# Kernel tuning notes

Measured on AMD Instinct MI355X. Metric: run time of the kernel, lower is better.

The kernel has to match this reference:

```python
import jax, jax.numpy as jnp
import numpy as np

NEG_INF = -1e30  # mask value used by QANet's apply_mask


def setup_inputs() -> dict:
    key = jax.random.key(0)
    ks = jax.random.split(key, 6)
    B, C, Q, H = 64, 1024, 128, 512
    return {
        "x_context": jax.random.normal(ks[0], (B, C, H), dtype=jnp.float32),
        "x_query": jax.random.normal(ks[1], (B, Q, H), dtype=jnp.float32),
        "context_mask": jnp.ones((B, C), dtype=jnp.float32),
        "query_mask": jnp.ones((B, Q), dtype=jnp.float32),
        "W0": jax.random.normal(ks[2], (H,), dtype=jnp.float32) * 0.05,
        "W1": jax.random.normal(ks[3], (H,), dtype=jnp.float32) * 0.05,
        "W2": jax.random.normal(ks[4], (H,), dtype=jnp.float32) * 0.05,
        "bias": jnp.zeros((1,), dtype=jnp.float32),
    }


def reference(x_context, x_query, context_mask, query_mask, W0, W1, W2, bias):
    # Trilinear similarity S[b,c,q] = q.W0 + c.W1 + (q*W2).c + bias
    # (original computes [B,Q,C] then transposes; we build [B,C,Q] directly)
    sub0 = jnp.einsum('bqh,h->bq', x_query, W0)          # [B,Q]
    sub1 = jnp.einsum('bch,h->bc', x_context, W1)        # [B,C]
    sub2 = jnp.einsum('bch,bqh->bcq', x_context, x_query * W2)  # [B,C,Q]
    S = sub2 + sub1[:, :, None] + sub0[:, None, :] + bias  # [B,C,Q]

    mq = query_mask[:, None, :]    # [B,1,Q]
    mc = context_mask[:, :, None]  # [B,C,1]

    # context-to-query: softmax over query axis, masked by query_mask
    S_ = jax.nn.softmax(S + (1.0 - mq) * NEG_INF, axis=-1)  # [B,C,Q]
    c2q = jnp.einsum('bcq,bqh->bch', S_, x_query)           # [B,C,H]

    # query-to-context: softmax over context axis, masked by context_mask
    S_c = jax.nn.softmax(S + (1.0 - mc) * NEG_INF, axis=1)  # [B,C,Q]
    S_T = jnp.swapaxes(S_c, 1, 2)                            # [B,Q,C]
    # (S_ @ S_T) @ x_context, associated as S_ @ (S_T @ x_context)
    tmp = jnp.einsum('bqc,bch->bqh', S_T, x_context)        # [B,Q,H]
    q2c = jnp.einsum('bcq,bqh->bch', S_, tmp)               # [B,C,H]
    return c2q, q2c
```

## Files before the change

### kernel.cpp

```cpp
#include <hip/hip_runtime.h>

#define BB 64
#define CC 1024
#define QQ 128
#define HH 512

typedef short bf16x8 __attribute__((ext_vector_type(8)));
typedef float f32x4 __attribute__((ext_vector_type(4)));

#define GLD16(g, l)                                                            \
    __builtin_amdgcn_global_load_lds(                                          \
        (const __attribute__((address_space(1))) unsigned int*)(g),            \
        (__attribute__((address_space(3))) unsigned int*)(l), 16, 0, 0)

__device__ __forceinline__ unsigned short f2bf(float f) {
    unsigned u = __float_as_uint(f);
    u += 0x7FFF + ((u >> 16) & 1);
    return (unsigned short)(u >> 16);
}
__device__ __forceinline__ unsigned pk2(float lo, float hi) {
    return (unsigned)f2bf(lo) | ((unsigned)f2bf(hi) << 16);
}

__global__ __launch_bounds__(256) void k_sub0(const float* __restrict__ xq,
                                              const float* __restrict__ w0,
                                              float* __restrict__ sub0,
                                              float* __restrict__ colsum) {
    if (blockIdx.x < 32) colsum[blockIdx.x * 256 + threadIdx.x] = 0.0f;
    int wave = threadIdx.x >> 6;
    int lane = threadIdx.x & 63;
    int row  = blockIdx.x * 4 + wave;
    const float* p = xq + (size_t)row * HH + lane * 8;
    float4 a0 = *(const float4*)(p);
    float4 a1 = *(const float4*)(p + 4);
    float4 b0 = *(const float4*)(w0 + lane * 8);
    float4 b1 = *(const float4*)(w0 + lane * 8 + 4);
    float s = a0.x*b0.x + a0.y*b0.y + a0.z*b0.z + a0.w*b0.w
            + a1.x*b1.x + a1.y*b1.y + a1.z*b1.z + a1.w*b1.w;
    #pragma unroll
    for (int off = 32; off; off >>= 1) s += __shfl_xor(s, off);
    if (lane == 0) sub0[row] = s;
}

__global__ __launch_bounds__(256) void k_prep(const float* __restrict__ xq,
                                              const float* __restrict__ w2,
                                              const float* __restrict__ qmask,
                                              unsigned short* __restrict__ xqw2b,
                                              unsigned short* __restrict__ xqmT) {
    int b  = blockIdx.y;
    int ht = blockIdx.x * 128;
    int tid = threadIdx.x;
    __shared__ __align__(16) unsigned short sT[128][132];

    {
        int q  = tid >> 1;
        int hh = (tid & 1) * 64;
        float qm = qmask[b * QQ + q];
        const float* xp = xq + ((size_t)b * QQ + q) * HH + ht + hh;
        unsigned short* wr = xqw2b + ((size_t)b * QQ + q) * HH + ht + hh;
        #pragma unroll
        for (int i = 0; i < 16; i++) {
            float4 v = *(const float4*)(xp + i * 4);
            float4 w = *(const float4*)(w2 + ht + hh + i * 4);
            uint2 pw; pw.x = pk2(v.x * w.x, v.y * w.y);
                      pw.y = pk2(v.z * w.z, v.w * w.w);
            *(uint2*)(wr + i * 4) = pw;
            uint2 pm; pm.x = pk2(v.x * qm, v.y * qm);
                      pm.y = pk2(v.z * qm, v.w * qm);
            *(uint2*)(&sT[q][hh + i * 4]) = pm;
        }
    }
    __syncthreads();
    {
        int h  = tid >> 1;
        int qh = (tid & 1) * 64;
        unsigned short* orow = xqmT + ((size_t)b * HH + ht + h) * QQ + qh;
        #pragma unroll
        for (int i = 0; i < 8; i++) {
            uint4 o;
            o.x = (unsigned)sT[qh + i*8 + 0][h] | ((unsigned)sT[qh + i*8 + 1][h] << 16);
            o.y = (unsigned)sT[qh + i*8 + 2][h] | ((unsigned)sT[qh + i*8 + 3][h] << 16);
            o.z = (unsigned)sT[qh + i*8 + 4][h] | ((unsigned)sT[qh + i*8 + 5][h] << 16);
            o.w = (unsigned)sT[qh + i*8 + 6][h] | ((unsigned)sT[qh + i*8 + 7][h] << 16);
            *(uint4*)(orow + i * 8) = o;
        }
    }
}

__global__ __launch_bounds__(256) void k_scores(
    const float* __restrict__ xc, const unsigned short* __restrict__ xqw2b,
    const float* __restrict__ w1, const float* __restrict__ cmask,
    const float* __restrict__ qmask, const float* __restrict__ bias,
    const float* __restrict__ sub0, unsigned short* __restrict__ Ebf,
    float* __restrict__ rowsum, float* __restrict__ colsum) {
    int b  = blockIdx.y;
    int c0 = blockIdx.x * 128;
    int tid  = threadIdx.x;
    int lane = tid & 63, wave = tid >> 6;
    int quad = lane >> 4, lcol = lane & 15;
    int wrow = (wave >> 1) * 64, wcol = (wave & 1) * 64;

    __shared__ __align__(16) unsigned short sA[128][32];
    __shared__ __align__(16) unsigned short sB[128][32];
    __shared__ float sW1[512];
    __shared__ float sSub1[128];
    __shared__ float sS0[128], sQm[128], sCm[128];
    __shared__ float sRowP[2][128], sColP[2][128];

    sW1[tid] = w1[tid]; sW1[tid + 256] = w1[tid + 256];
    if (tid < 128) {
        sS0[tid] = sub0[b * QQ + tid] + bias[0];
        sQm[tid] = qmask[b * QQ + tid];
        sCm[tid] = cmask[b * CC + c0 + tid];
    }

    f32x4 acc[4][4];
    #pragma unroll
    for (int i = 0; i < 4; i++)
        #pragma unroll
        for (int j = 0; j < 4; j++) acc[i][j] = (f32x4)0.0f;
    float s1 = 0.0f;

    int arow = tid >> 1, akh = (tid & 1) * 16;

    for (int k0 = 0; k0 < HH; k0 += 32) {
        __syncthreads();
        {
            const float* gp = xc + ((size_t)(b * CC + c0 + arow)) * HH + k0 + akh;
            float4 v0 = *(const float4*)(gp);
            float4 v1 = *(const float4*)(gp + 4);
            float4 v2 = *(const float4*)(gp + 8);
            float4 v3 = *(const float4*)(gp + 12);
            const float* wp = sW1 + k0 + akh;
            s1 += v0.x*wp[0] + v0.y*wp[1] + v0.z*wp[2] + v0.w*wp[3]
                + v1.x*wp[4] + v1.y*wp[5] + v1.z*wp[6] + v1.w*wp[7]
                + v2.x*wp[8] + v2.y*wp[9] + v2.z*wp[10] + v2.w*wp[11]
                + v3.x*wp[12] + v3.y*wp[13] + v3.z*wp[14] + v3.w*wp[15];
            uint4 p0, p1;
            p0.x = pk2(v0.x, v0.y); p0.y = pk2(v0.z, v0.w);
            p0.z = pk2(v1.x, v1.y); p0.w = pk2(v1.z, v1.w);
            p1.x = pk2(v2.x, v2.y); p1.y = pk2(v2.z, v2.w);
            p1.z = pk2(v3.x, v3.y); p1.w = pk2(v3.z, v3.w);
            *(uint4*)&sA[arow][akh]     = p0;
            *(uint4*)&sA[arow][akh + 8] = p1;
        }
        #pragma unroll
        for (int j = 0; j < 2; j++) {
            int chunk = wave * 2 + j;
            int row = chunk * 16 + (lane >> 2);
            GLD16(xqw2b + ((size_t)b * QQ + row) * HH + k0 + (lane & 3) * 8,
                  (unsigned short*)sB + chunk * 512);
        }
        __syncthreads();
        bf16x8 af[4];
        #pragma unroll
        for (int mi = 0; mi < 4; mi++)
            af[mi] = *(const bf16x8*)&sA[wrow + mi * 16 + lcol][quad * 8];
        #pragma unroll
        for (int ni = 0; ni < 4; ni++) {
            bf16x8 bfr = *(const bf16x8*)&sB[wcol + ni * 16 + lcol][quad * 8];
            #pragma unroll
            for (int mi = 0; mi < 4; mi++)
                acc[mi][ni] = __builtin_amdgcn_mfma_f32_16x16x32_bf16(
                    af[mi], bfr, acc[mi][ni], 0, 0, 0);
        }
    }

    s1 += __shfl_xor(s1, 1);
    if ((tid & 1) == 0) sSub1[arow] = s1;
    __syncthreads();

    float rsp[4][4];
    float csp[4] = {0.f, 0.f, 0.f, 0.f};
    #pragma unroll
    for (int mi = 0; mi < 4; mi++)
        #pragma unroll
        for (int r = 0; r < 4; r++) rsp[mi][r] = 0.f;

    #pragma unroll
    for (int mi = 0; mi < 4; mi++) {
        #pragma unroll
        for (int ni = 0; ni < 4; ni++) {
            int col = wcol + ni * 16 + lcol;
            float qm = sQm[col], s0 = sS0[col];
            #pragma unroll
            for (int r = 0; r < 4; r++) {
                int row = wrow + mi * 16 + quad * 4 + r;
                float e = __expf(acc[mi][ni][r] + sSub1[row] + s0);
                acc[mi][ni][r] = e;
                rsp[mi][r] += e * qm;
                csp[ni] += e * sCm[row];
            }
        }
    }
    #pragma unroll
    for (int mi = 0; mi < 4; mi++)
        #pragma unroll
        for (int r = 0; r < 4; r++) {
            float v = rsp[mi][r];
            v += __shfl_xor(v, 1); v += __shfl_xor(v, 2);
            v += __shfl_xor(v, 4); v += __shfl_xor(v, 8);
            if (lcol == 0) sRowP[wave & 1][wrow + mi * 16 + quad * 4 + r] = v;
        }
    #pragma unroll
    for (int ni = 0; ni < 4; ni++) {
        float v = csp[ni];
        v += __shfl_xor(v, 16); v += __shfl_xor(v, 32);
        if (quad == 0) sColP[wave >> 1][wcol + ni * 16 + lcol] = v;
    }
    #pragma unroll
    for (int mi = 0; mi < 4; mi++)
        #pragma unroll
        for (int ni = 0; ni < 4; ni++) {
            int col = wcol + ni * 16 + lcol;
            #pragma unroll
            for (int r = 0; r < 4; r++) {
                int row = wrow + mi * 16 + quad * 4 + r;
                Ebf[((size_t)(b * CC + c0 + row)) * QQ + col] = f2bf(acc[mi][ni][r]);
            }
        }
    __syncthreads();
    if (tid < 128) {
        rowsum[(size_t)b * CC + c0 + tid] = sRowP[0][tid] + sRowP[1][tid];
        atomicAdd(&colsum[b * QQ + tid], sColP[0][tid] + sColP[1][tid]);
    }
}

__global__ __launch_bounds__(256) void k_tmp(
    const unsigned short* __restrict__ Ebf, const float* __restrict__ xc,
    const float* __restrict__ cmask, const float* __restrict__ qmask,
    const float* __restrict__ colsum, unsigned short* __restrict__ tmpT) {
    int b  = blockIdx.y;
    int h0 = blockIdx.x * 64;
    int tid  = threadIdx.x;
    int lane = tid & 63, wave = tid >> 6;
    int quad = lane >> 4, lcol = lane & 15;
    int wrow = (wave >> 1) * 64;
    int wcol = (wave & 1) * 32;

    __shared__ __align__(16) unsigned int sAu[128 * 16];
    __shared__ __align__(16) unsigned int sBu[64 * 16];
    __shared__ float sInv[128];
    if (tid < 128) sInv[tid] = qmask[b * QQ + tid] / colsum[b * QQ + tid];

    f32x4 acc[4][2];
    #pragma unroll
    for (int i = 0; i < 4; i++) { acc[i][0] = (f32x4)0.f; acc[i][1] = (f32x4)0.f; }

    int tp = tid >> 4;
    int tq = tid & 15;

    for (int c0 = 0; c0 < CC; c0 += 32) {
        __syncthreads();
        {
            const unsigned short* ep = Ebf + ((size_t)b * CC + c0 + 2 * tp) * QQ + tq * 8;
            union { uint4 v; unsigned short s[8]; } r0, r1;
            r0.v = *(const uint4*)ep;
            r1.v = *(const uint4*)(ep + QQ);
            #pragma unroll
            for (int j = 0; j < 8; j++) {
                int q = tq * 8 + j;
                unsigned pk = (unsigned)r0.s[j] | ((unsigned)r1.s[j] << 16);
                sAu[q * 16 + (((tp >> 2) ^ (q >> 3 & 3)) << 2) + (tp & 3)] = pk;
            }
        }
        {
            const float* xp = xc + ((size_t)b * CC + c0 + 2 * tp) * HH + h0 + tq * 4;
            float cm0 = cmask[b * CC + c0 + 2 * tp];
            float cm1 = cmask[b * CC + c0 + 2 * tp + 1];
            float4 f0 = *(const float4*)xp;
            float4 f1 = *(const float4*)(xp + HH);
            float a0[4] = {f0.x, f0.y, f0.z, f0.w};
            float a1[4] = {f1.x, f1.y, f1.z, f1.w};
            #pragma unroll
            for (int j = 0; j < 4; j++) {
                int h = tq * 4 + j;
                unsigned pk = pk2(a0[j] * cm0, a1[j] * cm1);
                sBu[h * 16 + (((tp >> 2) ^ (h >> 3 & 3)) << 2) + (tp & 3)] = pk;
            }
        }
        __syncthreads();
        bf16x8 af[4];
        #pragma unroll
        for (int mi = 0; mi < 4; mi++) {
            int m = wrow + mi * 16 + lcol;
            af[mi] = *(const bf16x8*)(sAu + m * 16 + ((quad ^ (m >> 3 & 3)) << 2));
        }
        #pragma unroll
        for (int ni = 0; ni < 2; ni++) {
            int n = wcol + ni * 16 + lcol;
            bf16x8 bfr = *(const bf16x8*)(sBu + n * 16 + ((quad ^ (n >> 3 & 3)) << 2));
            #pragma unroll
            for (int mi = 0; mi < 4; mi++)
                acc[mi][ni] = __builtin_amdgcn_mfma_f32_16x16x32_bf16(
                    af[mi], bfr, acc[mi][ni], 0, 0, 0);
        }
    }
    #pragma unroll
    for (int mi = 0; mi < 4; mi++) {
        int qb = wrow + mi * 16 + quad * 4;
        #pragma unroll
        for (int ni = 0; ni < 2; ni++) {
            int h = wcol + ni * 16 + lcol;
            uint2 o;
            o.x = pk2(acc[mi][ni][0] * sInv[qb + 0], acc[mi][ni][1] * sInv[qb + 1]);
            o.y = pk2(acc[mi][ni][2] * sInv[qb + 2], acc[mi][ni][3] * sInv[qb + 3]);
            *(uint2*)(tmpT + ((size_t)b * HH + h0 + h) * QQ + qb) = o;
        }
    }
}

__global__ __launch_bounds__(256) void k_out(
    const unsigned short* __restrict__ Ebf, const unsigned short* __restrict__ xqmT,
    const unsigned short* __restrict__ tmpT, const float* __restrict__ rowsum,
    float* __restrict__ c2q, float* __restrict__ q2c) {
    int b  = blockIdx.z;
    int c0 = blockIdx.y * 128;
    int h0 = blockIdx.x * 128;
    int tid  = threadIdx.x;
    int lane = tid & 63, wave = tid >> 6;
    int quad = lane >> 4, lcol = lane & 15;
    int wrow = (wave >> 1) * 64, wcol = (wave & 1) * 64;

    __shared__ __align__(16) unsigned short sA[128][32];
    __shared__ __align__(16) unsigned short sB1[128][32];
    __shared__ __align__(16) unsigned short sB2[128][32];
    __shared__ float sInvR[128];
    if (tid < 128) sInvR[tid] = 1.0f / rowsum[(size_t)b * CC + c0 + tid];

    f32x4 acc1[4][4], acc2[4][4];
    #pragma unroll
    for (int i = 0; i < 4; i++)
        #pragma unroll
        for (int j = 0; j < 4; j++) { acc1[i][j] = (f32x4)0.f; acc2[i][j] = (f32x4)0.f; }

    for (int k0 = 0; k0 < QQ; k0 += 32) {
        __syncthreads();
        #pragma unroll
        for (int j = 0; j < 2; j++) {
            int chunk = wave * 2 + j;
            int row = chunk * 16 + (lane >> 2);
            int kb  = (lane & 3) * 8;
            GLD16(Ebf  + ((size_t)b * CC + c0 + row) * QQ + k0 + kb,
                  (unsigned short*)sA + chunk * 512);
            GLD16(xqmT + ((size_t)b * HH + h0 + row) * QQ + k0 + kb,
                  (unsigned short*)sB1 + chunk * 512);
            GLD16(tmpT + ((size_t)b * HH + h0 + row) * QQ + k0 + kb,
                  (unsigned short*)sB2 + chunk * 512);
        }
        __syncthreads();
        bf16x8 af[4];
        #pragma unroll
        for (int mi = 0; mi < 4; mi++)
            af[mi] = *(const bf16x8*)&sA[wrow + mi * 16 + lcol][quad * 8];
        #pragma unroll
        for (int ni = 0; ni < 4; ni++) {
            bf16x8 b1 = *(const bf16x8*)&sB1[wcol + ni * 16 + lcol][quad * 8];
            bf16x8 b2 = *(const bf16x8*)&sB2[wcol + ni * 16 + lcol][quad * 8];
            #pragma unroll
            for (int mi = 0; mi < 4; mi++) {
                acc1[mi][ni] = __builtin_amdgcn_mfma_f32_16x16x32_bf16(
                    af[mi], b1, acc1[mi][ni], 0, 0, 0);
                acc2[mi][ni] = __builtin_amdgcn_mfma_f32_16x16x32_bf16(
                    af[mi], b2, acc2[mi][ni], 0, 0, 0);
            }
        }
    }
    #pragma unroll
    for (int mi = 0; mi < 4; mi++) {
        int rb = wrow + mi * 16 + quad * 4;
        float ir0 = sInvR[rb], ir1 = sInvR[rb + 1], ir2 = sInvR[rb + 2], ir3 = sInvR[rb + 3];
        #pragma unroll
        for (int ni = 0; ni < 4; ni++) {
            int col = h0 + wcol + ni * 16 + lcol;
            size_t o0 = ((size_t)b * CC + c0 + rb) * HH + col;
            c2q[o0]          = acc1[mi][ni][0] * ir0;
            c2q[o0 + HH]     = acc1[mi][ni][1] * ir1;
            c2q[o0 + 2*HH]   = acc1[mi][ni][2] * ir2;
            c2q[o0 + 3*HH]   = acc1[mi][ni][3] * ir3;
            q2c[o0]          = acc2[mi][ni][0] * ir0;
            q2c[o0 + HH]     = acc2[mi][ni][1] * ir1;
            q2c[o0 + 2*HH]   = acc2[mi][ni][2] * ir2;
            q2c[o0 + 3*HH]   = acc2[mi][ni][3] * ir3;
        }
    }
}

extern "C" void kernel_launch(void* const* d_in, const int* in_sizes, int n_in,
                              void* d_out, int out_size, void* d_ws, size_t ws_size,
                              hipStream_t stream) {
    const float* xc    = (const float*)d_in[0];
    const float* xq    = (const float*)d_in[1];
    const float* cmask = (const float*)d_in[2];
    const float* qmask = (const float*)d_in[3];
    const float* w0    = (const float*)d_in[4];
    const float* w1    = (const float*)d_in[5];
    const float* w2    = (const float*)d_in[6];
    const float* bias  = (const float*)d_in[7];

    float* out = (float*)d_out;
    float* c2q = out;
    float* q2c = out + (size_t)BB * CC * HH;

    unsigned short* Ebf   = (unsigned short*)d_ws;
    unsigned short* xqw2b = Ebf   + (size_t)BB * CC * QQ;
    unsigned short* xqmT  = xqw2b + (size_t)BB * QQ * HH;
    unsigned short* tmpT  = xqmT  + (size_t)BB * QQ * HH;
    float* rowsum = (float*)(tmpT + (size_t)BB * QQ * HH);
    float* colsum = rowsum + (size_t)BB * CC;
    float* sub0   = colsum + (size_t)BB * QQ;

    k_sub0  <<<dim3(BB * QQ / 4),      256, 0, stream>>>(xq, w0, sub0, colsum);
    k_prep  <<<dim3(HH / 128, BB),     256, 0, stream>>>(xq, w2, qmask, xqw2b, xqmT);
    k_scores<<<dim3(CC / 128, BB),     256, 0, stream>>>(xc, xqw2b, w1, cmask, qmask,
                                                         bias, sub0, Ebf, rowsum, colsum);
    k_tmp   <<<dim3(HH / 64, BB),      256, 0, stream>>>(Ebf, xc, cmask, qmask,
                                                         colsum, tmpT);
    k_out   <<<dim3(HH / 128, CC / 128, BB), 256, 0, stream>>>(Ebf, xqmT, tmpT,
                                                               rowsum, c2q, q2c);
}
```

Before: 474.9 us.

## Double-buffer LDS tiles in scores, tmp and output GEMM kernels

Converts the main K-loops of k_scores, k_tmp and k_out to a two-stage ping-pong LDS pipeline. The next tile's global loads (register loads or global_load_lds) are issued before the MFMA work on the current tile, and one barrier per iteration replaces two. The aim is to hide global memory latency behind the matrix math. In exchange, LDS usage doubles and register pressure rises from holding the prefetched values, which could lower occupancy.

```diff
diff --git a/kernel.cpp b/kernel.cpp
--- a/kernel.cpp
+++ b/kernel.cpp
@@ -100,8 +100,8 @@
     int quad = lane >> 4, lcol = lane & 15;
     int wrow = (wave >> 1) * 64, wcol = (wave & 1) * 64;
 
-    __shared__ __align__(16) unsigned short sA[128][32];
-    __shared__ __align__(16) unsigned short sB[128][32];
+    __shared__ __align__(16) unsigned short sA[2][128][32];
+    __shared__ __align__(16) unsigned short sB[2][128][32];
     __shared__ float sW1[512];
     __shared__ float sSub1[128];
     __shared__ float sS0[128], sQm[128], sCm[128];
@@ -122,16 +122,70 @@
     float s1 = 0.0f;
 
     int arow = tid >> 1, akh = (tid & 1) * 16;
-
-    for (int k0 = 0; k0 < HH; k0 += 32) {
-        __syncthreads();
-        {
-            const float* gp = xc + ((size_t)(b * CC + c0 + arow)) * HH + k0 + akh;
-            float4 v0 = *(const float4*)(gp);
-            float4 v1 = *(const float4*)(gp + 4);
-            float4 v2 = *(const float4*)(gp + 8);
-            float4 v3 = *(const float4*)(gp + 12);
-            const float* wp = sW1 + k0 + akh;
+    const float* gbase = xc + ((size_t)(b * CC + c0 + arow)) * HH + akh;
+
+    __syncthreads();
+
+    {
+        float4 v0 = *(const float4*)(gbase);
+        float4 v1 = *(const float4*)(gbase + 4);
+        float4 v2 = *(const float4*)(gbase + 8);
+        float4 v3 = *(const float4*)(gbase + 12);
+        const float* wp = sW1 + akh;
+        s1 += v0.x*wp[0] + v0.y*wp[1] + v0.z*wp[2] + v0.w*wp[3]
+            + v1.x*wp[4] + v1.y*wp[5] + v1.z*wp[6] + v1.w*wp[7]
+            + v2.x*wp[8] + v2.y*wp[9] + v2.z*wp[10] + v2.w*wp[11]
+            + v3.x*wp[12] + v3.y*wp[13] + v3.z*wp[14] + v3.w*wp[15];
+        uint4 p0, p1;
+        p0.x = pk2(v0.x, v0.y); p0.y = pk2(v0.z, v0.w);
+        p0.z = pk2(v1.x, v1.y); p0.w = pk2(v1.z, v1.w);
+        p1.x = pk2(v2.x, v2.y); p1.y = pk2(v2.z, v2.w);
+        p1.z = pk2(v3.x, v3.y); p1.w = pk2(v3.z, v3.w);
+        *(uint4*)&sA[0][arow][akh]     = p0;
+        *(uint4*)&sA[0][arow][akh + 8] = p1;
+    }
+    #pragma unroll
+    for (int j = 0; j < 2; j++) {
+        int chunk = wave * 2 + j;
+        int row = chunk * 16 + (lane >> 2);
+        GLD16(xqw2b + ((size_t)b * QQ + row) * HH + (lane & 3) * 8,
+              (unsigned short*)sB[0] + chunk * 512);
+    }
+    __syncthreads();
+
+    for (int t = 0; t < 16; ++t) {
+        int cur = t & 1, alt = cur ^ 1;
+        bool pf = (t < 15);
+        int kn = (t + 1) * 32;
+        float4 v0, v1, v2, v3;
+        if (pf) {
+            const float* gp = gbase + kn;
+            v0 = *(const float4*)(gp);
+            v1 = *(const float4*)(gp + 4);
+            v2 = *(const float4*)(gp + 8);
+            v3 = *(const float4*)(gp + 12);
+            #pragma unroll
+            for (int j = 0; j < 2; j++) {
+                int chunk = wave * 2 + j;
+                int row = chunk * 16 + (lane >> 2);
+                GLD16(xqw2b + ((size_t)b * QQ + row) * HH + kn + (lane & 3) * 8,
+                      (unsigned short*)sB[alt] + chunk * 512);
+            }
+        }
+        bf16x8 af[4];
+        #pragma unroll
+        for (int mi = 0; mi < 4; mi++)
+            af[mi] = *(const bf16x8*)&sA[cur][wrow + mi * 16 + lcol][quad * 8];
+        #pragma unroll
+        for (int ni = 0; ni < 4; ni++) {
+            bf16x8 bfr = *(const bf16x8*)&sB[cur][wcol + ni * 16 + lcol][quad * 8];
+            #pragma unroll
+            for (int mi = 0; mi < 4; mi++)
+                acc[mi][ni] = __builtin_amdgcn_mfma_f32_16x16x32_bf16(
+                    af[mi], bfr, acc[mi][ni], 0, 0, 0);
+        }
+        if (pf) {
+            const float* wp = sW1 + kn + akh;
             s1 += v0.x*wp[0] + v0.y*wp[1] + v0.z*wp[2] + v0.w*wp[3]
                 + v1.x*wp[4] + v1.y*wp[5] + v1.z*wp[6] + v1.w*wp[7]
                 + v2.x*wp[8] + v2.y*wp[9] + v2.z*wp[10] + v2.w*wp[11]
@@ -141,29 +195,10 @@
             p0.z = pk2(v1.x, v1.y); p0.w = pk2(v1.z, v1.w);
             p1.x = pk2(v2.x, v2.y); p1.y = pk2(v2.z, v2.w);
             p1.z = pk2(v3.x, v3.y); p1.w = pk2(v3.z, v3.w);
-            *(uint4*)&sA[arow][akh]     = p0;
-            *(uint4*)&sA[arow][akh + 8] = p1;
-        }
-        #pragma unroll
-        for (int j = 0; j < 2; j++) {
-            int chunk = wave * 2 + j;
-            int row = chunk * 16 + (lane >> 2);
-            GLD16(xqw2b + ((size_t)b * QQ + row) * HH + k0 + (lane & 3) * 8,
-                  (unsigned short*)sB + chunk * 512);
+            *(uint4*)&sA[alt][arow][akh]     = p0;
+            *(uint4*)&sA[alt][arow][akh + 8] = p1;
         }
         __syncthreads();
-        bf16x8 af[4];
-        #pragma unroll
-        for (int mi = 0; mi < 4; mi++)
-            af[mi] = *(const bf16x8*)&sA[wrow + mi * 16 + lcol][quad * 8];
-        #pragma unroll
-        for (int ni = 0; ni < 4; ni++) {
-            bf16x8 bfr = *(const bf16x8*)&sB[wcol + ni * 16 + lcol][quad * 8];
-            #pragma unroll
-            for (int mi = 0; mi < 4; mi++)
-                acc[mi][ni] = __builtin_amdgcn_mfma_f32_16x16x32_bf16(
-                    af[mi], bfr, acc[mi][ni], 0, 0, 0);
-        }
     }
 
     s1 += __shfl_xor(s1, 1);
@@ -238,8 +273,8 @@
     int wrow = (wave >> 1) * 64;
     int wcol = (wave & 1) * 32;
 
-    __shared__ __align__(16) unsigned int sAu[128 * 16];
-    __shared__ __align__(16) unsigned int sBu[64 * 16];
+    __shared__ __align__(16) unsigned int sAu[2][128 * 16];
+    __shared__ __align__(16) unsigned int sBu[2][64 * 16];
     __shared__ float sInv[128];
     if (tid < 128) sInv[tid] = qmask[b * QQ + tid] / colsum[b * QQ + tid];
 
@@ -250,51 +285,82 @@
     int tp = tid >> 4;
     int tq = tid & 15;
 
-    for (int c0 = 0; c0 < CC; c0 += 32) {
-        __syncthreads();
-        {
-            const unsigned short* ep = Ebf + ((size_t)b * CC + c0 + 2 * tp) * QQ + tq * 8;
-            union { uint4 v; unsigned short s[8]; } r0, r1;
-            r0.v = *(const uint4*)ep;
-            r1.v = *(const uint4*)(ep + QQ);
+    const unsigned short* ebase = Ebf + ((size_t)b * CC + 2 * tp) * QQ + tq * 8;
+    const float*          xbase = xc  + ((size_t)b * CC + 2 * tp) * HH + h0 + tq * 4;
+    const float*          mbase = cmask + (size_t)b * CC + 2 * tp;
+
+    {
+        union { uint4 v; unsigned short s[8]; } r0, r1;
+        r0.v = *(const uint4*)(ebase);
+        r1.v = *(const uint4*)(ebase + QQ);
+        float cm0 = mbase[0];
+        float cm1 = mbase[1];
+        float4 f0 = *(const float4*)(xbase);
+        float4 f1 = *(const float4*)(xbase + HH);
+        #pragma unroll
+        for (int j = 0; j < 8; j++) {
+            int q = tq * 8 + j;
+            unsigned pk = (unsigned)r0.s[j] | ((unsigned)r1.s[j] << 16);
+            sAu[0][q * 16 + (((tp >> 2) ^ (q >> 3 & 3)) << 2) + (tp & 3)] = pk;
+        }
+        float a0[4] = {f0.x, f0.y, f0.z, f0.w};
+        float a1[4] = {f1.x, f1.y, f1.z, f1.w};
+        #pragma unroll
+        for (int j = 0; j < 4; j++) {
+            int h = tq * 4 + j;
+            unsigned pk = pk2(a0[j] * cm0, a1[j] * cm1);
+            sBu[0][h * 16 + (((tp >> 2) ^ (h >> 3 & 3)) << 2) + (tp & 3)] = pk;
+        }
+    }
+    __syncthreads();
+
+    for (int t = 0; t < 32; ++t) {
+        int cur = t & 1, alt = cur ^ 1;
+        bool pf = (t < 31);
+        int cn = (t + 1) * 32;
+        union { uint4 v; unsigned short s[8]; } r0, r1;
+        float4 f0, f1;
+        float cm0, cm1;
+        if (pf) {
+            r0.v = *(const uint4*)(ebase + (size_t)cn * QQ);
+            r1.v = *(const uint4*)(ebase + (size_t)cn * QQ + QQ);
+            cm0 = mbase[cn];
+            cm1 = mbase[cn + 1];
+            f0 = *(const float4*)(xbase + (size_t)cn * HH);
+            f1 = *(const float4*)(xbase + (size_t)cn * HH + HH);
+        }
+        bf16x8 af[4];
+        #pragma unroll
+        for (int mi = 0; mi < 4; mi++) {
+            int m = wrow + mi * 16 + lcol;
+            af[mi] = *(const bf16x8*)(sAu[cur] + m * 16 + ((quad ^ (m >> 3 & 3)) << 2));
+        }
+        #pragma unroll
+        for (int ni = 0; ni < 2; ni++) {
+            int n = wcol + ni * 16 + lcol;
+            bf16x8 bfr = *(const bf16x8*)(sBu[cur] + n * 16 + ((quad ^ (n >> 3 & 3)) << 2));
+            #pragma unroll
+            for (int mi = 0; mi < 4; mi++)
+                acc[mi][ni] = __builtin_amdgcn_mfma_f32_16x16x32_bf16(
+                    af[mi], bfr, acc[mi][ni], 0, 0, 0);
+        }
+        if (pf) {
             #pragma unroll
             for (int j = 0; j < 8; j++) {
                 int q = tq * 8 + j;
                 unsigned pk = (unsigned)r0.s[j] | ((unsigned)r1.s[j] << 16);
-                sAu[q * 16 + (((tp >> 2) ^ (q >> 3 & 3)) << 2) + (tp & 3)] = pk;
-            }
-        }
-        {
-            const float* xp = xc + ((size_t)b * CC + c0 + 2 * tp) * HH + h0 + tq * 4;
-            float cm0 = cmask[b * CC + c0 + 2 * tp];
-            float cm1 = cmask[b * CC + c0 + 2 * tp + 1];
-            float4 f0 = *(const float4*)xp;
-            float4 f1 = *(const float4*)(xp + HH);
+                sAu[alt][q * 16 + (((tp >> 2) ^ (q >> 3 & 3)) << 2) + (tp & 3)] = pk;
+            }
             float a0[4] = {f0.x, f0.y, f0.z, f0.w};
             float a1[4] = {f1.x, f1.y, f1.z, f1.w};
             #pragma unroll
             for (int j = 0; j < 4; j++) {
                 int h = tq * 4 + j;
                 unsigned pk = pk2(a0[j] * cm0, a1[j] * cm1);
-                sBu[h * 16 + (((tp >> 2) ^ (h >> 3 & 3)) << 2) + (tp & 3)] = pk;
+                sBu[alt][h * 16 + (((tp >> 2) ^ (h >> 3 & 3)) << 2) + (tp & 3)] = pk;
             }
         }
         __syncthreads();
-        bf16x8 af[4];
-        #pragma unroll
-        for (int mi = 0; mi < 4; mi++) {
-            int m = wrow + mi * 16 + lcol;
-            af[mi] = *(const bf16x8*)(sAu + m * 16 + ((quad ^ (m >> 3 & 3)) << 2));
-        }
-        #pragma unroll
-        for (int ni = 0; ni < 2; ni++) {
-            int n = wcol + ni * 16 + lcol;
-            bf16x8 bfr = *(const bf16x8*)(sBu + n * 16 + ((quad ^ (n >> 3 & 3)) << 2));
-            #pragma unroll
-            for (int mi = 0; mi < 4; mi++)
-                acc[mi][ni] = __builtin_amdgcn_mfma_f32_16x16x32_bf16(
-                    af[mi], bfr, acc[mi][ni], 0, 0, 0);
-        }
     }
     #pragma unroll
     for (int mi = 0; mi < 4; mi++) {
@@ -322,9 +388,9 @@
     int quad = lane >> 4, lcol = lane & 15;
     int wrow = (wave >> 1) * 64, wcol = (wave & 1) * 64;
 
-    __shared__ __align__(16) unsigned short sA[128][32];
-    __shared__ __align__(16) unsigned short sB1[128][32];
-    __shared__ __align__(16) unsigned short sB2[128][32];
+    __shared__ __align__(16) unsigned short sA[2][128][32];
+    __shared__ __align__(16) unsigned short sB1[2][128][32];
+    __shared__ __align__(16) unsigned short sB2[2][128][32];
     __shared__ float sInvR[128];
     if (tid < 128) sInvR[tid] = 1.0f / rowsum[(size_t)b * CC + c0 + tid];
 
@@ -334,29 +400,46 @@
         #pragma unroll
         for (int j = 0; j < 4; j++) { acc1[i][j] = (f32x4)0.f; acc2[i][j] = (f32x4)0.f; }
 
-    for (int k0 = 0; k0 < QQ; k0 += 32) {
-        __syncthreads();
-        #pragma unroll
-        for (int j = 0; j < 2; j++) {
-            int chunk = wave * 2 + j;
-            int row = chunk * 16 + (lane >> 2);
-            int kb  = (lane & 3) * 8;
-            GLD16(Ebf  + ((size_t)b * CC + c0 + row) * QQ + k0 + kb,
-                  (unsigned short*)sA + chunk * 512);
-            GLD16(xqmT + ((size_t)b * HH + h0 + row) * QQ + k0 + kb,
-                  (unsigned short*)sB1 + chunk * 512);
-            GLD16(tmpT + ((size_t)b * HH + h0 + row) * QQ + k0 + kb,
-                  (unsigned short*)sB2 + chunk * 512);
-        }
-        __syncthreads();
+    #pragma unroll
+    for (int j = 0; j < 2; j++) {
+        int chunk = wave * 2 + j;
+        int row = chunk * 16 + (lane >> 2);
+        int kb  = (lane & 3) * 8;
+        GLD16(Ebf  + ((size_t)b * CC + c0 + row) * QQ + kb,
+              (unsigned short*)sA[0] + chunk * 512);
+        GLD16(xqmT + ((size_t)b * HH + h0 + row) * QQ + kb,
+              (unsigned short*)sB1[0] + chunk * 512);
+        GLD16(tmpT + ((size_t)b * HH + h0 + row) * QQ + kb,
+              (unsigned short*)sB2[0] + chunk * 512);
+    }
+    __syncthreads();
+
+    for (int t = 0; t < 4; ++t) {
+        int cur = t & 1, alt = cur ^ 1;
+        bool pf = (t < 3);
+        int kn = (t + 1) * 32;
+        if (pf) {
+            #pragma unroll
+            for (int j = 0; j < 2; j++) {
+                int chunk = wave * 2 + j;
+                int row = chunk * 16 + (lane >> 2);
+                int kb  = (lane & 3) * 8;
+                GLD16(Ebf  + ((size_t)b * CC + c0 + row) * QQ + kn + kb,
+                      (unsigned short*)sA[alt] + chunk * 512);
+                GLD16(xqmT + ((size_t)b * HH + h0 + row) * QQ + kn + kb,
+                      (unsigned short*)sB1[alt] + chunk * 512);
+                GLD16(tmpT + ((size_t)b * HH + h0 + row) * QQ + kn + kb,
+                      (unsigned short*)sB2[alt] + chunk * 512);
+            }
+        }
         bf16x8 af[4];
         #pragma unroll
         for (int mi = 0; mi < 4; mi++)
-            af[mi] = *(const bf16x8*)&sA[wrow + mi * 16 + lcol][quad * 8];
+            af[mi] = *(const bf16x8*)&sA[cur][wrow + mi * 16 + lcol][quad * 8];
         #pragma unroll
         for (int ni = 0; ni < 4; ni++) {
-            bf16x8 b1 = *(const bf16x8*)&sB1[wcol + ni * 16 + lcol][quad * 8];
-            bf16x8 b2 = *(const bf16x8*)&sB2[wcol + ni * 16 + lcol][quad * 8];
+            bf16x8 b1 = *(const bf16x8*)&sB1[cur][wcol + ni * 16 + lcol][quad * 8];
+            bf16x8 b2 = *(const bf16x8*)&sB2[cur][wcol + ni * 16 + lcol][quad * 8];
             #pragma unroll
             for (int mi = 0; mi < 4; mi++) {
                 acc1[mi][ni] = __builtin_amdgcn_mfma_f32_16x16x32_bf16(
@@ -365,6 +448,7 @@
                     af[mi], b2, acc2[mi][ni], 0, 0, 0);
             }
         }
+        __syncthreads();
     }
     #pragma unroll
     for (int mi = 0; mi < 4; mi++) {
```

New measurement: 483.7 us. About the same (+1.8%).
